# Kernel tuning notes

Hardware: AMD Instinct MI355X
Metric: run time of the kernel (lower is better)

Reference implementation:

```python
import jax, jax.numpy as jnp
import numpy as np

NUM_HEADS = 16  # concat repeats the identical head output this many times


def setup_inputs() -> dict:
    key = jax.random.key(0)
    ks = jax.random.split(key, 6)
    B, S, E, D = 4, 4096, 1024, 64  # D = E // NUM_HEADS
    s_in = 1.0 / np.sqrt(E)
    return {
        "x": jax.random.normal(ks[0], (B, S, E), dtype=jnp.float32),
        "Wq": jax.random.normal(ks[1], (E, D), dtype=jnp.float32) * s_in,
        "bq": jnp.zeros((D,), dtype=jnp.float32),
        "Wk": jax.random.normal(ks[2], (E, D), dtype=jnp.float32) * s_in,
        "bk": jnp.zeros((D,), dtype=jnp.float32),
        "Wv": jax.random.normal(ks[3], (E, D), dtype=jnp.float32) * s_in,
        "bv": jnp.zeros((D,), dtype=jnp.float32),
        "Wo": jax.random.normal(ks[4], (E, E), dtype=jnp.float32) * s_in,
        "bo": jnp.zeros((E,), dtype=jnp.float32),
    }


def reference(x, Wq, bq, Wk, bk, Wv, bv, Wo, bo):
    # Single shared projection to head_dim (the torch code projects E -> E//H once).
    q = x @ Wq + bq          # [B,S,D]
    k = x @ Wk + bk          # [B,S,D]
    v = x @ Wv + bv          # [B,S,D]
    d = q.shape[-1]
    scale = 1.0 / jnp.sqrt(jnp.asarray(d, dtype=q.dtype))
    scores = jnp.einsum("bqd,bkd->bqk", q, k) * scale   # [B,S,S]
    attn = jax.nn.softmax(scores, axis=-1)
    ctx = jnp.einsum("bqk,bkd->bqd", attn, v)            # [B,S,D]
    # Every head computes the identical result; concat == tile along features.
    cat = jnp.tile(ctx, (1, 1, NUM_HEADS))               # [B,S,E]
    return cat @ Wo + bo
```

## Files before the change

kernel.cpp:

```cpp
#include <hip/hip_runtime.h>
#include <hip/hip_bf16.h>

#define BB 4
#define SS 4096
#define EE 1024
#define DD 64

typedef unsigned short u16;
typedef unsigned int   u32;
typedef __bf16 bf16_t;
typedef bf16_t bf16x2 __attribute__((ext_vector_type(2)));
typedef bf16_t bf16x8 __attribute__((ext_vector_type(8)));
typedef float  f32x4  __attribute__((ext_vector_type(4)));
typedef u32    u32x4  __attribute__((ext_vector_type(4)));

__device__ __forceinline__ u16 f2bf_hw(float f) {
    bf16_t b = (bf16_t)f;
    u16 u; __builtin_memcpy(&u, &b, 2);
    return u;
}

__global__ __launch_bounds__(256) void wt_kernel(const float* __restrict__ Wq,
                                                 const float* __restrict__ Wk,
                                                 const float* __restrict__ Wv,
                                                 u16* __restrict__ Wt) {
    int t = blockIdx.x * 256 + threadIdx.x;
    int c = t >> 10, e = t & 1023;
    const float* W = (c < 64) ? Wq : (c < 128) ? Wk : Wv;
    Wt[c * 1024 + e] = f2bf_hw(W[e * 64 + (c & 63)]);
}

__global__ __launch_bounds__(256) void wosum_kernel(const float* __restrict__ Wo,
                                                    float* __restrict__ WoSum) {
    int t = blockIdx.x * 256 + threadIdx.x;
    int d = t >> 10, e = t & 1023;
    float s = 0.f;
    #pragma unroll
    for (int h = 0; h < 16; h++) s += Wo[(h * 64 + d) * 1024 + e];
    WoSum[t] = s;
}

__global__ __launch_bounds__(256) void proj_kernel(const float* __restrict__ x,
                                                   const u16* __restrict__ Wtg,
                                                   const float* __restrict__ bq,
                                                   const float* __restrict__ bk,
                                                   const float* __restrict__ bv,
                                                   u16* __restrict__ Qg,
                                                   u16* __restrict__ Kg,
                                                   u16* __restrict__ Vtg) {
    __shared__ __align__(16) u16 xt[32 * 136];
    __shared__ __align__(16) u16 wts[192 * 136];

    const int tid  = threadIdx.x;
    const int w    = tid >> 6;
    const int lane = tid & 63;
    const int m    = lane & 15;
    const int quad = lane >> 4;
    const int r0   = blockIdx.x * 32;
    const int mt   = w & 1;
    const int ch   = w >> 1;

    f32x4 acc[6];
    #pragma unroll
    for (int i = 0; i < 6; i++) acc[i] = (f32x4){0.f, 0.f, 0.f, 0.f};

    f32x4 xr[4];
    u32x4 wr[12];

    auto preload = [&](int kb) {
        #pragma unroll
        for (int j = 0; j < 2; j++) {
            const int id = tid + j * 256, row = id >> 4, seg = id & 15;
            const float* src = x + (r0 + row) * 1024 + kb * 128 + seg * 8;
            xr[2 * j]     = *(const f32x4*)(src);
            xr[2 * j + 1] = *(const f32x4*)(src + 4);
        }
        #pragma unroll
        for (int j = 0; j < 12; j++) {
            const int id = tid + j * 256, row = id >> 4, seg = id & 15;
            wr[j] = *(const u32x4*)(Wtg + row * 1024 + kb * 128 + seg * 8);
        }
    };
    auto commit = [&]() {
        #pragma unroll
        for (int j = 0; j < 2; j++) {
            const int id = tid + j * 256, row = id >> 4, seg = id & 15;
            bf16x8 v;
            #pragma unroll
            for (int k = 0; k < 4; k++) {
                v[k]     = (bf16_t)xr[2 * j][k];
                v[4 + k] = (bf16_t)xr[2 * j + 1][k];
            }
            *(bf16x8*)(xt + row * 136 + seg * 8) = v;
        }
        #pragma unroll
        for (int j = 0; j < 12; j++) {
            const int id = tid + j * 256, row = id >> 4, seg = id & 15;
            *(u32x4*)(wts + row * 136 + seg * 8) = wr[j];
        }
    };

    preload(0);
    for (int kb = 0; kb < 8; kb++) {
        __syncthreads();
        commit();
        __syncthreads();
        if (kb < 7) preload(kb + 1);
        #pragma unroll
        for (int ks = 0; ks < 4; ks++) {
            bf16x8 a = *(const bf16x8*)(xt + (mt * 16 + m) * 136 + ks * 32 + quad * 8);
            #pragma unroll
            for (int c = 0; c < 6; c++) {
                bf16x8 b = *(const bf16x8*)(wts + (ch * 96 + c * 16 + m) * 136 + ks * 32 + quad * 8);
                acc[c] = __builtin_amdgcn_mfma_f32_16x16x32_bf16(a, b, acc[c], 0, 0, 0);
            }
        }
    }

    const int rbase = r0 + mt * 16 + quad * 4;
    #pragma unroll
    for (int c = 0; c < 6; c++) {
        const int col   = ch * 96 + c * 16 + m;
        const int which = col >> 6;
        const int d     = col & 63;
        const float bias = (which == 0 ? bq : which == 1 ? bk : bv)[d];
        #pragma unroll
        for (int r = 0; r < 4; r++) {
            const int row = rbase + r;
            float v = acc[c][r] + bias;
            if (which == 0) {
                Qg[row * 64 + d] = f2bf_hw(v * 0.125f);
            } else if (which == 1) {
                Kg[row * 64 + d] = f2bf_hw(v);
            } else {
                const int b = row >> 12, s = row & 4095;
                const int sp = (s & ~31) | ((s & 12) << 1) | (s & 3) | ((s >> 2) & 4);
                Vtg[(b * 64 + d) * 4096 + sp] = f2bf_hw(v);
            }
        }
    }
}

#define ATTN_LDS 73728
__global__ __launch_bounds__(512) void attn_kernel(const u16* __restrict__ Qg,
                                                   const u16* __restrict__ Kg,
                                                   const u16* __restrict__ Vtg,
                                                   float* __restrict__ ctxP,
                                                   float* __restrict__ liP) {
    extern __shared__ __align__(16) u16 smem[];

    const int tid  = threadIdx.x;
    const int w    = tid >> 6;
    const int lane = tid & 63;
    const int m    = lane & 15;
    const int quad = lane >> 4;
    const int kg   = w >> 1;
    const int qg   = w & 1;

    const int bi    = blockIdx.x;
    const int khalf = bi & 1;
    const int batch = (bi >> 1) & 3;
    const int qt    = bi >> 3;
    const int qrow0 = batch * 4096 + qt * 64;

    bf16x8 aq[2][2];
    #pragma unroll
    for (int s = 0; s < 2; s++) {
        const int qr = qrow0 + qg * 32 + s * 16 + m;
        aq[s][0] = *(const bf16x8*)(Qg + qr * 64 + quad * 8);
        aq[s][1] = *(const bf16x8*)(Qg + qr * 64 + 32 + quad * 8);
    }

    f32x4 acc[2][4];
    float li[2] = {0.f, 0.f};
    #pragma unroll
    for (int s = 0; s < 2; s++)
        #pragma unroll
        for (int c = 0; c < 4; c++) acc[s][c] = (f32x4){0.f, 0.f, 0.f, 0.f};

    const u16* Kbase = Kg + (batch * 4096 + khalf * 2048) * 64;
    const u16* Vbase = Vtg + batch * 64 * 4096 + khalf * 2048;

    const int krow = qg * 16 + (lane >> 3);
    const int kseg = lane & 7;
    const int kxor = (lane >> 3) & 7;
    const int vrow = qg * 32 + (lane >> 2);
    const int vseg = lane & 3;

    u32x4 kr[2], vr[2];
    auto preload = [&](int it) {
        const int k0 = it * 128 + kg * 32;
        #pragma unroll
        for (int i = 0; i < 2; i++) {
            kr[i] = *(const u32x4*)(Kbase + (k0 + krow + 8 * i) * 64 + kseg * 8);
            vr[i] = *(const u32x4*)(Vbase + (vrow + 16 * i) * 4096 + k0 + vseg * 8);
        }
    };
    auto commit = [&](u16* Kt, u16* Vt) {
        #pragma unroll
        for (int i = 0; i < 2; i++) {
            *(u32x4*)(Kt + (krow + 8 * i) * 64 + ((kseg ^ kxor) * 8)) = kr[i];
            *(u32x4*)(Vt + (vrow + 16 * i) * 40 + vseg * 8) = vr[i];
        }
    };

    const float LOG2E = 1.4426950408889634f;
    const float NC2   = -12.0f * 1.4426950408889634f;

    preload(0);
    {
        u16* base = smem + kg * 4608;
        commit(base, base + 2048);
    }
    __syncthreads();

    for (int it = 0; it < 16; it++) {
        const int cur = it & 1;
        u16* Kt = smem + cur * 18432 + kg * 4608;
        u16* Vt = Kt + 2048;

        if (it < 15) preload(it + 1);

        f32x4 sc[2][2];
        #pragma unroll
        for (int c = 0; c < 2; c++) {
            const int row = c * 16 + m;
            bf16x8 k0f = *(const bf16x8*)(Kt + row * 64 + ((quad ^ (m & 7)) * 8));
            bf16x8 k1f = *(const bf16x8*)(Kt + row * 64 + (((quad | 4) ^ (m & 7)) * 8));
            #pragma unroll
            for (int s = 0; s < 2; s++) {
                f32x4 t = __builtin_amdgcn_mfma_f32_16x16x32_bf16(k0f, aq[s][0], (f32x4){0.f,0.f,0.f,0.f}, 0, 0, 0);
                sc[s][c] = __builtin_amdgcn_mfma_f32_16x16x32_bf16(k1f, aq[s][1], t, 0, 0, 0);
            }
        }

        bf16x8 pa[2];
        #pragma unroll
        for (int s = 0; s < 2; s++) {
            float p[8];
            #pragma unroll
            for (int r = 0; r < 4; r++) {
                p[r]     = __builtin_exp2f(__builtin_fmaf(sc[s][0][r], LOG2E, NC2));
                p[4 + r] = __builtin_exp2f(__builtin_fmaf(sc[s][1][r], LOG2E, NC2));
            }
            li[s] += ((p[0] + p[1]) + (p[2] + p[3])) + ((p[4] + p[5]) + (p[6] + p[7]));
            #pragma unroll
            for (int j = 0; j < 8; j++) pa[s][j] = (bf16_t)p[j];
        }

        #pragma unroll
        for (int c = 0; c < 4; c++) {
            bf16x8 bv = *(const bf16x8*)(Vt + (c * 16 + m) * 40 + quad * 8);
            #pragma unroll
            for (int s = 0; s < 2; s++)
                acc[s][c] = __builtin_amdgcn_mfma_f32_16x16x32_bf16(pa[s], bv, acc[s][c], 0, 0, 0);
        }

        if (it < 15) {
            u16* Kn = smem + (cur ^ 1) * 18432 + kg * 4608;
            commit(Kn, Kn + 2048);
        }
        __syncthreads();
    }

    #pragma unroll
    for (int s = 0; s < 2; s++) {
        float v = li[s];
        v += __shfl_xor(v, 16);
        v += __shfl_xor(v, 32);
        li[s] = v;
    }

    float* mf = (float*)smem;
    float* cb = mf + w * 2208;
    #pragma unroll
    for (int s = 0; s < 2; s++)
        #pragma unroll
        for (int c = 0; c < 4; c++)
            #pragma unroll
            for (int r = 0; r < 4; r++)
                cb[(s * 16 + quad * 4 + r) * 68 + c * 16 + m] = acc[s][c][r];
    if (lane < 16) {
        #pragma unroll
        for (int s = 0; s < 2; s++) cb[2176 + s * 16 + m] = li[s];
    }
    __syncthreads();

    const int q  = tid >> 3;
    const int d0 = (tid & 7) * 8;
    const int qgq = q >> 5;
    const int ql  = q & 31;
    float L = 0.f;
    f32x4 o0 = (f32x4){0.f, 0.f, 0.f, 0.f};
    f32x4 o1 = (f32x4){0.f, 0.f, 0.f, 0.f};
    #pragma unroll
    for (int g = 0; g < 4; g++) {
        const float* c2 = mf + (g * 2 + qgq) * 2208;
        L  += c2[2176 + ql];
        o0 += *(const f32x4*)(c2 + ql * 68 + d0);
        o1 += *(const f32x4*)(c2 + ql * 68 + d0 + 4);
    }
    const int gr = khalf * 16384 + qrow0 + q;
    *(f32x4*)(ctxP + gr * 64 + d0)     = o0;
    *(f32x4*)(ctxP + gr * 64 + d0 + 4) = o1;
    if ((tid & 7) == 0) liP[gr] = L;
}

__global__ __launch_bounds__(256) void out_kernel(const float* __restrict__ ctxP,
                                                  const float* __restrict__ liP,
                                                  const float* __restrict__ WoSum,
                                                  const float* __restrict__ bo,
                                                  float* __restrict__ out) {
    __shared__ float cl[64 * 64];
    __shared__ float linv[64];
    const int tid = threadIdx.x;
    const int r0  = (blockIdx.x >> 2) * 64;
    const int eb  = (blockIdx.x & 3) * 256;

    if (tid < 64) {
        linv[tid] = 1.0f / (liP[r0 + tid] + liP[16384 + r0 + tid]);
    }
    const float* A = ctxP + r0 * 64;
    const float* B = ctxP + 16384 * 64 + r0 * 64;
    #pragma unroll
    for (int j = 0; j < 4; j++) {
        const int pos = (tid + j * 256) * 4;
        f32x4 a4 = *(const f32x4*)(A + pos);
        f32x4 b4 = *(const f32x4*)(B + pos);
        *(f32x4*)(cl + pos) = a4 + b4;
    }
    __syncthreads();

    const int rg = tid >> 6;
    const int cg = tid & 63;
    const int e0 = eb + cg * 4;

    f32x4 a[16];
    #pragma unroll
    for (int r = 0; r < 16; r++) a[r] = (f32x4){0.f, 0.f, 0.f, 0.f};

    for (int d = 0; d < 64; d++) {
        f32x4 wv = *(const f32x4*)(WoSum + d * 1024 + e0);
        #pragma unroll
        for (int r = 0; r < 16; r++) {
            a[r] += wv * cl[(rg * 16 + r) * 64 + d];
        }
    }
    f32x4 bo4 = *(const f32x4*)(bo + e0);
    #pragma unroll
    for (int r = 0; r < 16; r++) {
        f32x4 o = a[r] * linv[rg * 16 + r] + bo4;
        *(f32x4*)(out + (r0 + rg * 16 + r) * 1024 + e0) = o;
    }
}

extern "C" void kernel_launch(void* const* d_in, const int* in_sizes, int n_in,
                              void* d_out, int out_size, void* d_ws, size_t ws_size,
                              hipStream_t stream) {
    const float* x  = (const float*)d_in[0];
    const float* Wq = (const float*)d_in[1];
    const float* bq = (const float*)d_in[2];
    const float* Wk = (const float*)d_in[3];
    const float* bk = (const float*)d_in[4];
    const float* Wv = (const float*)d_in[5];
    const float* bv = (const float*)d_in[6];
    const float* Wo = (const float*)d_in[7];
    const float* bo = (const float*)d_in[8];
    float* out = (float*)d_out;

    char* ws = (char*)d_ws;
    u16*   Wt   = (u16*)(ws);
    float* WoS  = (float*)(ws + 393216);
    u16*   Qg   = (u16*)(ws + 655360);
    u16*   Kg   = (u16*)(ws + 2752512);
    u16*   Vtg  = (u16*)(ws + 4849664);
    float* ctxP = (float*)(ws + 6946816);
    float* liP  = (float*)(ws + 15335424);

    (void)hipFuncSetAttribute((const void*)attn_kernel,
                              hipFuncAttributeMaxDynamicSharedMemorySize, ATTN_LDS);

    wt_kernel   <<<768,  256, 0, stream>>>(Wq, Wk, Wv, Wt);
    wosum_kernel<<<256,  256, 0, stream>>>(Wo, WoS);
    proj_kernel <<<512,  256, 0, stream>>>(x, Wt, bq, bk, bv, Qg, Kg, Vtg);
    attn_kernel <<<512,  512, ATTN_LDS, stream>>>(Qg, Kg, Vtg, ctxP, liP);
    out_kernel  <<<1024, 256, 0, stream>>>(ctxP, liP, WoS, bo, out);
}
```

Measured before the change: 206.7 us.

## Use split-bf16 MFMA for output projection and merge weight prep kernels

Replaces the fp32 FMA loop in the output projection with bf16 MFMA instructions. Accuracy is kept by splitting both the normalized context and the head-summed Wo into high and low bf16 parts and computing three cross products. The two weight-preparation kernels are merged into one launch that also writes a transposed hi/lo copy of WoSum. This trades extra MFMA work and scattered scalar output stores for moving the fp32 ALU-bound GEMM onto matrix cores and saving one launch.

```diff
diff --git a/kernel.cpp b/kernel.cpp
--- a/kernel.cpp
+++ b/kernel.cpp
@@ -19,25 +19,51 @@
     u16 u; __builtin_memcpy(&u, &b, 2);
     return u;
 }
-
-__global__ __launch_bounds__(256) void wt_kernel(const float* __restrict__ Wq,
-                                                 const float* __restrict__ Wk,
-                                                 const float* __restrict__ Wv,
-                                                 u16* __restrict__ Wt) {
-    int t = blockIdx.x * 256 + threadIdx.x;
-    int c = t >> 10, e = t & 1023;
-    const float* W = (c < 64) ? Wq : (c < 128) ? Wk : Wv;
-    Wt[c * 1024 + e] = f2bf_hw(W[e * 64 + (c & 63)]);
-}
-
-__global__ __launch_bounds__(256) void wosum_kernel(const float* __restrict__ Wo,
-                                                    float* __restrict__ WoSum) {
-    int t = blockIdx.x * 256 + threadIdx.x;
-    int d = t >> 10, e = t & 1023;
-    float s = 0.f;
-    #pragma unroll
-    for (int h = 0; h < 16; h++) s += Wo[(h * 64 + d) * 1024 + e];
-    WoSum[t] = s;
+__device__ __forceinline__ void bfsplit(float v, u16& h, u16& l) {
+    bf16_t hb = (bf16_t)v;
+    float hf = (float)hb;
+    __builtin_memcpy(&h, &hb, 2);
+    bf16_t lb = (bf16_t)(v - hf);
+    __builtin_memcpy(&l, &lb, 2);
+}
+
+__global__ __launch_bounds__(256) void prep_kernel(const float* __restrict__ Wq,
+                                                   const float* __restrict__ Wk,
+                                                   const float* __restrict__ Wv,
+                                                   const float* __restrict__ Wo,
+                                                   u16* __restrict__ Wt,
+                                                   u16* __restrict__ WoTh,
+                                                   u16* __restrict__ WoTl) {
+    __shared__ float sm[64 * 65];
+    const int b = blockIdx.x;
+    const int tid = threadIdx.x;
+    if (b < 768) {
+        int t = b * 256 + tid;
+        int c = t >> 10, e = t & 1023;
+        const float* W = (c < 64) ? Wq : (c < 128) ? Wk : Wv;
+        Wt[c * 1024 + e] = f2bf_hw(W[e * 64 + (c & 63)]);
+        return;
+    }
+    const int eb = (b - 768) * 64;
+    #pragma unroll
+    for (int j = 0; j < 16; j++) {
+        const int idx = j * 256 + tid;
+        const int d = idx >> 6, el = idx & 63;
+        float s = 0.f;
+        #pragma unroll
+        for (int h = 0; h < 16; h++) s += Wo[(h * 64 + d) * 1024 + eb + el];
+        sm[d * 65 + el] = s;
+    }
+    __syncthreads();
+    #pragma unroll
+    for (int j = 0; j < 16; j++) {
+        const int idx = j * 256 + tid;
+        const int el = idx >> 6, d = idx & 63;
+        u16 h, l;
+        bfsplit(sm[d * 65 + el], h, l);
+        WoTh[(eb + el) * 64 + d] = h;
+        WoTl[(eb + el) * 64 + d] = l;
+    }
 }
 
 __global__ __launch_bounds__(256) void proj_kernel(const float* __restrict__ x,
@@ -308,49 +334,97 @@
 
 __global__ __launch_bounds__(256) void out_kernel(const float* __restrict__ ctxP,
                                                   const float* __restrict__ liP,
-                                                  const float* __restrict__ WoSum,
+                                                  const u16* __restrict__ WoTh,
+                                                  const u16* __restrict__ WoTl,
                                                   const float* __restrict__ bo,
                                                   float* __restrict__ out) {
-    __shared__ float cl[64 * 64];
-    __shared__ float linv[64];
+    __shared__ __align__(16) u16 ldsH[64 * 72];
+    __shared__ __align__(16) u16 ldsL[64 * 72];
     const int tid = threadIdx.x;
     const int r0  = (blockIdx.x >> 2) * 64;
     const int eb  = (blockIdx.x & 3) * 256;
 
-    if (tid < 64) {
-        linv[tid] = 1.0f / (liP[r0 + tid] + liP[16384 + r0 + tid]);
-    }
-    const float* A = ctxP + r0 * 64;
-    const float* B = ctxP + 16384 * 64 + r0 * 64;
-    #pragma unroll
-    for (int j = 0; j < 4; j++) {
-        const int pos = (tid + j * 256) * 4;
-        f32x4 a4 = *(const f32x4*)(A + pos);
-        f32x4 b4 = *(const f32x4*)(B + pos);
-        *(f32x4*)(cl + pos) = a4 + b4;
+    {
+        const int q  = tid >> 2;
+        const int dq = (tid & 3) * 16;
+        const float inv = 1.0f / (liP[r0 + q] + liP[16384 + r0 + q]);
+        const float* A = ctxP + (r0 + q) * 64 + dq;
+        const float* B = ctxP + 16384 * 64 + (r0 + q) * 64 + dq;
+        #pragma unroll
+        for (int i = 0; i < 4; i++) {
+            f32x4 a4 = *(const f32x4*)(A + i * 4);
+            f32x4 b4 = *(const f32x4*)(B + i * 4);
+            f32x4 o  = (a4 + b4) * inv;
+            u16 h[4], l[4];
+            #pragma unroll
+            for (int k = 0; k < 4; k++) bfsplit(o[k], h[k], l[k]);
+            u32 h0 = (u32)h[0] | ((u32)h[1] << 16);
+            u32 h1 = (u32)h[2] | ((u32)h[3] << 16);
+            u32 l0 = (u32)l[0] | ((u32)l[1] << 16);
+            u32 l1 = (u32)l[2] | ((u32)l[3] << 16);
+            const int off = q * 72 + dq + i * 4;
+            *(u32*)(ldsH + off)     = h0;
+            *(u32*)(ldsH + off + 2) = h1;
+            *(u32*)(ldsL + off)     = l0;
+            *(u32*)(ldsL + off + 2) = l1;
+        }
     }
     __syncthreads();
 
-    const int rg = tid >> 6;
-    const int cg = tid & 63;
-    const int e0 = eb + cg * 4;
-
-    f32x4 a[16];
-    #pragma unroll
-    for (int r = 0; r < 16; r++) a[r] = (f32x4){0.f, 0.f, 0.f, 0.f};
-
-    for (int d = 0; d < 64; d++) {
-        f32x4 wv = *(const f32x4*)(WoSum + d * 1024 + e0);
-        #pragma unroll
-        for (int r = 0; r < 16; r++) {
-            a[r] += wv * cl[(rg * 16 + r) * 64 + d];
-        }
-    }
-    f32x4 bo4 = *(const f32x4*)(bo + e0);
-    #pragma unroll
-    for (int r = 0; r < 16; r++) {
-        f32x4 o = a[r] * linv[rg * 16 + r] + bo4;
-        *(f32x4*)(out + (r0 + rg * 16 + r) * 1024 + e0) = o;
+    const int w    = tid >> 6;
+    const int lane = tid & 63;
+    const int m    = lane & 15;
+    const int quad = lane >> 4;
+    const int wr   = w >> 1;
+    const int wc   = w & 1;
+
+    bf16x8 aH[2][2], aL[2][2];
+    #pragma unroll
+    for (int rs = 0; rs < 2; rs++)
+        #pragma unroll
+        for (int ks = 0; ks < 2; ks++) {
+            const int off = (wr * 32 + rs * 16 + m) * 72 + ks * 32 + quad * 8;
+            aH[rs][ks] = *(const bf16x8*)(ldsH + off);
+            aL[rs][ks] = *(const bf16x8*)(ldsL + off);
+        }
+
+    f32x4 acc[2][8];
+    #pragma unroll
+    for (int rs = 0; rs < 2; rs++)
+        #pragma unroll
+        for (int cs = 0; cs < 8; cs++) acc[rs][cs] = (f32x4){0.f, 0.f, 0.f, 0.f};
+
+    #pragma unroll
+    for (int cs = 0; cs < 8; cs++) {
+        const int e = eb + wc * 128 + cs * 16 + m;
+        bf16x8 bh0 = *(const bf16x8*)(WoTh + e * 64 + quad * 8);
+        bf16x8 bh1 = *(const bf16x8*)(WoTh + e * 64 + 32 + quad * 8);
+        bf16x8 bl0 = *(const bf16x8*)(WoTl + e * 64 + quad * 8);
+        bf16x8 bl1 = *(const bf16x8*)(WoTl + e * 64 + 32 + quad * 8);
+        #pragma unroll
+        for (int rs = 0; rs < 2; rs++) {
+            f32x4 t = acc[rs][cs];
+            t = __builtin_amdgcn_mfma_f32_16x16x32_bf16(aH[rs][0], bh0, t, 0, 0, 0);
+            t = __builtin_amdgcn_mfma_f32_16x16x32_bf16(aH[rs][1], bh1, t, 0, 0, 0);
+            t = __builtin_amdgcn_mfma_f32_16x16x32_bf16(aL[rs][0], bh0, t, 0, 0, 0);
+            t = __builtin_amdgcn_mfma_f32_16x16x32_bf16(aL[rs][1], bh1, t, 0, 0, 0);
+            t = __builtin_amdgcn_mfma_f32_16x16x32_bf16(aH[rs][0], bl0, t, 0, 0, 0);
+            t = __builtin_amdgcn_mfma_f32_16x16x32_bf16(aH[rs][1], bl1, t, 0, 0, 0);
+            acc[rs][cs] = t;
+        }
+    }
+
+    #pragma unroll
+    for (int cs = 0; cs < 8; cs++) {
+        const int e = eb + wc * 128 + cs * 16 + m;
+        const float bov = bo[e];
+        #pragma unroll
+        for (int rs = 0; rs < 2; rs++) {
+            const int row = r0 + wr * 32 + rs * 16 + quad * 4;
+            #pragma unroll
+            for (int r = 0; r < 4; r++)
+                out[(row + r) * 1024 + e] = acc[rs][cs][r] + bov;
+        }
     }
 }
 
@@ -370,7 +444,8 @@
 
     char* ws = (char*)d_ws;
     u16*   Wt   = (u16*)(ws);
-    float* WoS  = (float*)(ws + 393216);
+    u16*   WoTh = (u16*)(ws + 393216);
+    u16*   WoTl = (u16*)(ws + 524288);
     u16*   Qg   = (u16*)(ws + 655360);
     u16*   Kg   = (u16*)(ws + 2752512);
     u16*   Vtg  = (u16*)(ws + 4849664);
@@ -380,9 +455,8 @@
     (void)hipFuncSetAttribute((const void*)attn_kernel,
                               hipFuncAttributeMaxDynamicSharedMemorySize, ATTN_LDS);
 
-    wt_kernel   <<<768,  256, 0, stream>>>(Wq, Wk, Wv, Wt);
-    wosum_kernel<<<256,  256, 0, stream>>>(Wo, WoS);
+    prep_kernel <<<784,  256, 0, stream>>>(Wq, Wk, Wv, Wo, Wt, WoTh, WoTl);
     proj_kernel <<<512,  256, 0, stream>>>(x, Wt, bq, bk, bv, Qg, Kg, Vtg);
     attn_kernel <<<512,  512, ATTN_LDS, stream>>>(Qg, Kg, Vtg, ctxP, liP);
-    out_kernel  <<<1024, 256, 0, stream>>>(ctxP, liP, WoS, bo, out);
-}
+    out_kernel  <<<1024, 256, 0, stream>>>(ctxP, liP, WoTh, WoTl, bo, out);
+}
```

Result: slower. 276.1 us (+33.6%).
